# Kernel optimization log

Measured on AMD Instinct MI355X. Metric: run time of the kernel, lower is better.

## Reference

```python
import jax, jax.numpy as jnp
import numpy as np

B, N, K = 4, 8192, 24
D_POINTS, D_MODEL, PE_DIM = 32, 64, 60


def _sincos_embed(pos, embed_dim):
    # 3D sincos embedding: embed_dim//3 dims per axis, half sin half cos.
    d = embed_dim // 3                                   # 20 per axis
    omega = 1.0 / (10000.0 ** (jnp.arange(d // 2, dtype=jnp.float32) / (d / 2.0)))
    ang = pos[..., None] * omega                         # [..., 3, d//2]
    emb = jnp.concatenate([jnp.sin(ang), jnp.cos(ang)], axis=-1)  # [..., 3, d]
    return emb.reshape(pos.shape[:-1] + (embed_dim,))    # [..., 60]


def _knn_idx(xyz, k):
    # squared pairwise distances [B,N,N]; top_k(-d) == argsort(d)[:k]
    sq = jnp.sum(xyz * xyz, axis=-1)
    dists = sq[:, :, None] + sq[:, None, :] - 2.0 * jnp.einsum('bnc,bmc->bnm', xyz, xyz)
    _, idx = jax.lax.top_k(-dists, k)
    return idx                                           # [B,N,K] int32


def _gather(points, idx):
    # index_points: points [B,N,C], idx [B,N,K] -> [B,N,K,C]
    return jax.vmap(lambda p, i: p[i])(points, idx)


def setup_inputs():
    key = jax.random.key(0)
    ks = jax.random.split(key, 12)
    s = 0.02
    DK = D_MODEL * K
    return {
        'features': jax.random.normal(ks[0], (B, N, D_POINTS), jnp.float32),
        'xyz': jax.random.uniform(ks[1], (B, N, 3), jnp.float32),
        'W1': jax.random.normal(ks[2], (D_MODEL, D_POINTS), jnp.float32) * s,
        'b1': jnp.zeros((D_MODEL,), jnp.float32),
        'W2': jax.random.normal(ks[3], (D_MODEL, D_MODEL), jnp.float32) * s,
        'b2': jnp.zeros((D_MODEL,), jnp.float32),
        'Wd1': jax.random.normal(ks[4], (D_MODEL, PE_DIM), jnp.float32) * s,
        'bd1': jnp.zeros((D_MODEL,), jnp.float32),
        'Wd2': jax.random.normal(ks[5], (D_MODEL, D_MODEL), jnp.float32) * s,
        'bd2': jnp.zeros((D_MODEL,), jnp.float32),
        'Wa': jax.random.normal(ks[6], (DK, DK), jnp.float32) * s,
        'ba': jnp.zeros((DK,), jnp.float32),
    }


def reference(features, xyz, W1, b1, W2, b2, Wd1, bd1, Wd2, bd2, Wa, ba):
    knn_idx = _knn_idx(xyz, K)                # no-grad in original
    knn_xyz = _gather(xyz, knn_idx)           # [B,N,K,3]
    x = features @ W1.T + b1                  # fc1 -> [B,N,D]
    q = x
    kf = _gather(x, knn_idx)                  # [B,N,K,D]
    vf = kf
    g_xyz = xyz[:, :, None, :] - knn_xyz      # [B,N,K,3]
    pe = _sincos_embed(g_xyz, PE_DIM)         # [B,N,K,60]
    pos_enc = jnp.maximum(pe @ Wd1.T + bd1, 0.0) @ Wd2.T + bd2  # fc_delta
    pre = (q[:, :, None, :] - kf + pos_enc).reshape(B, N, K * D_MODEL)
    attn = (pre @ Wa.T + ba).reshape(B, N, K, D_MODEL)          # fc_atten
    attn = jax.nn.softmax(attn / np.float32(np.sqrt(D_MODEL)), axis=-2)
    res = jnp.einsum('bmnf,bmnf->bmf', attn, vf + pos_enc)
    res = res @ W2.T + b2 + x                 # fc2 + residual
    return res, attn
```

## Files before the change

kernel.cpp:

```cpp
#include <hip/hip_runtime.h>
#include <hip/hip_bf16.h>
#include <stdint.h>

#define BATCH 4
#define NPTS  8192
#define KNN   24
#define DPT   32
#define DM    64
#define PED   60
#define DK    (DM*KNN)
#define ROWS  (BATCH*NPTS)

#define GRIDN 16
#define NCELL (GRIDN*GRIDN*GRIDN)
#define CH    0.0625f

typedef __attribute__((ext_vector_type(8))) short short8;
typedef __attribute__((ext_vector_type(4))) float f32x4;
typedef __attribute__((address_space(3))) unsigned lds_u32;
typedef const __attribute__((address_space(1))) unsigned gbl_u32;

#define WSYNC() __builtin_amdgcn_wave_barrier()

static __device__ __forceinline__ unsigned short f2bf(float f) {
  __hip_bfloat16 h = __float2bfloat16(f);
  return *(unsigned short*)&h;
}
static __device__ __forceinline__ float bf2f(unsigned short u) {
  return __uint_as_float(((unsigned)u) << 16);
}

static __device__ __forceinline__ int cell_coord(float p) {
  int c = (int)(p * (float)GRIDN);
  c = (c < 0) ? 0 : c;
  c = (c > GRIDN - 1) ? GRIDN - 1 : c;
  return c;
}

__global__ __launch_bounds__(256) void fc1_kernel(
    const float* __restrict__ f, const float* __restrict__ W1,
    const float* __restrict__ b1, float* __restrict__ x) {
  int gid = blockIdx.x * 256 + threadIdx.x;
  int n = gid >> 6, c = gid & 63;
  const float* fr = f + (size_t)n * DPT;
  const float* wr = W1 + c * DPT;
  float acc = b1[c];
#pragma unroll
  for (int i = 0; i < DPT; ++i) acc = fmaf(fr[i], wr[i], acc);
  x[(size_t)n * DM + c] = acc;
}

__global__ __launch_bounds__(256) void grid_build_kernel(
    const float* __restrict__ xyz, int* __restrict__ cellStart,
    int* __restrict__ sortedIdx) {
  __shared__ int cnt[NCELL];
  __shared__ int partial[256];
  int b = blockIdx.x, tid = threadIdx.x;
  const float* P = xyz + (size_t)b * NPTS * 3;

  for (int i = tid; i < NCELL; i += 256) cnt[i] = 0;
  __syncthreads();
  for (int i = tid; i < NPTS; i += 256) {
    int cx = cell_coord(P[3 * i + 0]);
    int cy = cell_coord(P[3 * i + 1]);
    int cz = cell_coord(P[3 * i + 2]);
    atomicAdd(&cnt[(cx << 8) | (cy << 4) | cz], 1);
  }
  __syncthreads();
  int base = tid * 16, s = 0;
#pragma unroll
  for (int j = 0; j < 16; ++j) s += cnt[base + j];
  partial[tid] = s;
  __syncthreads();
  if (tid == 0) {
    int acc = 0;
    for (int i = 0; i < 256; ++i) { int v = partial[i]; partial[i] = acc; acc += v; }
  }
  __syncthreads();
  int acc = partial[tid];
#pragma unroll
  for (int j = 0; j < 16; ++j) {
    int c = cnt[base + j];
    cnt[base + j] = acc;
    cellStart[b * (NCELL + 1) + base + j] = acc;
    acc += c;
  }
  if (tid == 255) cellStart[b * (NCELL + 1) + NCELL] = NPTS;
  __syncthreads();
  for (int i = tid; i < NPTS; i += 256) {
    int cx = cell_coord(P[3 * i + 0]);
    int cy = cell_coord(P[3 * i + 1]);
    int cz = cell_coord(P[3 * i + 2]);
    int pos = atomicAdd(&cnt[(cx << 8) | (cy << 4) | cz], 1);
    sortedIdx[b * NPTS + pos] = i;
  }
}

__global__ __launch_bounds__(64) void grid_knn_kernel(
    const float* __restrict__ xyz, const int* __restrict__ cellStart,
    const int* __restrict__ sortedIdx, int* __restrict__ knn) {
  int t = blockIdx.x * 64 + threadIdx.x;
  int b = t >> 13, j = t & 8191;
  const int* cs = cellStart + b * (NCELL + 1);
  const int* si = sortedIdx + b * NPTS;
  const float* P = xyz + (size_t)b * NPTS * 3;

  int q = si[j];
  int n = (b << 13) + q;
  float qx = P[3 * q + 0], qy = P[3 * q + 1], qz = P[3 * q + 2];
  int cx = cell_coord(qx), cy = cell_coord(qy), cz = cell_coord(qz);

  unsigned long long key[KNN];
#pragma unroll
  for (int o = 0; o < KNN; ++o) key[o] = 0x7F800000FFFFFFFFULL;
  float lim = __builtin_inff();

  for (int rho = 0; rho <= GRIDN - 1; ++rho) {
    for (int dz = -rho; dz <= rho; ++dz) {
      int iz = cz + dz;
      if ((unsigned)iz >= GRIDN) continue;
      bool zface = (dz == -rho) || (dz == rho);
      for (int dy = -rho; dy <= rho; ++dy) {
        int iy = cy + dy;
        if ((unsigned)iy >= GRIDN) continue;
        bool face = zface || (dy == -rho) || (dy == rho);
        int dxstep = (rho == 0 || face) ? 1 : (2 * rho);
        for (int dx = -rho; dx <= rho; dx += dxstep) {
          int ix = cx + dx;
          if ((unsigned)ix >= GRIDN) continue;
          float bx = ix * CH, by = iy * CH, bz = iz * CH;
          float ex = fmaxf(fmaxf(bx - qx, qx - (bx + CH)), 0.f);
          float ey = fmaxf(fmaxf(by - qy, qy - (by + CH)), 0.f);
          float ez = fmaxf(fmaxf(bz - qz, qz - (bz + CH)), 0.f);
          float dsq = ex * ex + ey * ey + ez * ez;
          if (dsq * 0.99999f >= lim) continue;
          int cid = (ix << 8) | (iy << 4) | iz;
          int s0 = cs[cid], s1 = cs[cid + 1];
          for (int ii = s0; ii < s1; ++ii) {
            int m = si[ii];
            float ddx = qx - P[3 * m + 0];
            float ddy = qy - P[3 * m + 1];
            float ddz = qz - P[3 * m + 2];
            double dd = (double)ddx * (double)ddx + (double)ddy * (double)ddy
                      + (double)ddz * (double)ddz;
            float df = (float)dd;
            if (df < lim) {
              unsigned long long v =
                  ((unsigned long long)__float_as_uint(df) << 32) | (unsigned)m;
#pragma unroll
              for (int tt = 0; tt < KNN; ++tt) {
                bool take = v < key[tt];
                unsigned long long old = key[tt];
                key[tt] = take ? v : key[tt];
                v = take ? old : v;
              }
              lim = __uint_as_float((unsigned)(key[KNN - 1] >> 32));
            }
          }
        }
      }
    }
    float rb = rho * CH;
    if (lim < rb * rb * 0.999999f) break;
  }
#pragma unroll
  for (int o = 0; o < KNN; ++o)
    knn[(size_t)n * KNN + o] = (int)(unsigned)key[o];
}

__device__ __forceinline__ float pe_elem(int t, float gx, float gy, float gz) {
  const float OM[10] = {1.0f, 0.3981071705534972f, 0.15848931924611134f,
                        0.06309573444801933f, 0.025118864315095794f, 0.01f,
                        0.003981071705534973f, 0.001584893192461114f,
                        0.0006309573444801933f, 0.00025118864315095795f};
  int a = t / 20, r = t % 20;
  float g = (a == 0) ? gx : ((a == 1) ? gy : gz);
  float ang = g * OM[r % 10];
  return (r < 10) ? __sinf(ang) : __cosf(ang);
}

static __device__ __forceinline__ void pe_fill(
    unsigned short* scr, const float* __restrict__ xyz, const int* idxArr,
    int base, float qx, float qy, float qz, int ln) {
  for (int k = 0; k < KNN; ++k) {
    int gidx = base + idxArr[k];
    float gx = qx - xyz[(size_t)gidx * 3 + 0];
    float gy = qy - xyz[(size_t)gidx * 3 + 1];
    float gz = qz - xyz[(size_t)gidx * 3 + 2];
    float v = (ln < PED) ? pe_elem(ln, gx, gy, gz) : 0.f;
    scr[(k * 64 + ln) ^ ((k & 7) << 3)] = f2bf(v);
  }
#pragma unroll
  for (int k = KNN; k < 32; ++k)
    scr[(k * 64 + ln) ^ ((k & 7) << 3)] = 0;
  WSYNC();
}

static __device__ __forceinline__ short8 lds_read8(const unsigned short* p) {
  return *(const short8*)p;
}

static __device__ __forceinline__ void mlp_wave(
    unsigned short* scr, const unsigned short* w1b, const unsigned short* w2b,
    const float* __restrict__ bd1, const float* __restrict__ bd2, int ln) {
  int lrow = ln & 15, lq = ln >> 4;
  short8 af[2][2], bfr[4][2];
  f32x4 acc[2][4];

#pragma unroll
  for (int mt = 0; mt < 2; ++mt)
#pragma unroll
    for (int ks = 0; ks < 2; ++ks) {
      int row = mt * 16 + lrow;
      af[mt][ks] = lds_read8(scr + ((row * 64 + ks * 32 + lq * 8) ^ ((row & 7) << 3)));
    }
#pragma unroll
  for (int nt = 0; nt < 4; ++nt)
#pragma unroll
    for (int ks = 0; ks < 2; ++ks) {
      int row = nt * 16 + lrow;
      bfr[nt][ks] = lds_read8(w1b + ((row * 64 + ks * 32 + lq * 8) ^ ((row & 7) << 3)));
    }
#pragma unroll
  for (int mt = 0; mt < 2; ++mt)
#pragma unroll
    for (int nt = 0; nt < 4; ++nt) {
      f32x4 a = (f32x4){0.f, 0.f, 0.f, 0.f};
      a = __builtin_amdgcn_mfma_f32_16x16x32_bf16(af[mt][0], bfr[nt][0], a, 0, 0, 0);
      a = __builtin_amdgcn_mfma_f32_16x16x32_bf16(af[mt][1], bfr[nt][1], a, 0, 0, 0);
      acc[mt][nt] = a;
    }
  WSYNC();
#pragma unroll
  for (int mt = 0; mt < 2; ++mt)
#pragma unroll
    for (int nt = 0; nt < 4; ++nt) {
      float b1v = bd1[nt * 16 + lrow];
#pragma unroll
      for (int r = 0; r < 4; ++r) {
        int row = mt * 16 + lq * 4 + r;
        int col = nt * 16 + lrow;
        scr[(row * 64 + col) ^ ((row & 7) << 3)] =
            f2bf(fmaxf(acc[mt][nt][r] + b1v, 0.f));
      }
    }
  WSYNC();
#pragma unroll
  for (int mt = 0; mt < 2; ++mt)
#pragma unroll
    for (int ks = 0; ks < 2; ++ks) {
      int row = mt * 16 + lrow;
      af[mt][ks] = lds_read8(scr + ((row * 64 + ks * 32 + lq * 8) ^ ((row & 7) << 3)));
    }
#pragma unroll
  for (int nt = 0; nt < 4; ++nt)
#pragma unroll
    for (int ks = 0; ks < 2; ++ks) {
      int row = nt * 16 + lrow;
      bfr[nt][ks] = lds_read8(w2b + ((row * 64 + ks * 32 + lq * 8) ^ ((row & 7) << 3)));
    }
#pragma unroll
  for (int mt = 0; mt < 2; ++mt)
#pragma unroll
    for (int nt = 0; nt < 4; ++nt) {
      f32x4 a = (f32x4){0.f, 0.f, 0.f, 0.f};
      a = __builtin_amdgcn_mfma_f32_16x16x32_bf16(af[mt][0], bfr[nt][0], a, 0, 0, 0);
      a = __builtin_amdgcn_mfma_f32_16x16x32_bf16(af[mt][1], bfr[nt][1], a, 0, 0, 0);
      acc[mt][nt] = a;
    }
  WSYNC();
#pragma unroll
  for (int mt = 0; mt < 2; ++mt)
#pragma unroll
    for (int nt = 0; nt < 4; ++nt) {
      float b2v = bd2[nt * 16 + lrow];
#pragma unroll
      for (int r = 0; r < 4; ++r) {
        int row = mt * 16 + lq * 4 + r;
        int col = nt * 16 + lrow;
        scr[row * 68 + col] = f2bf(acc[mt][nt][r] + b2v);
      }
    }
  WSYNC();
}

__global__ __launch_bounds__(256) void prebuild_kernel(
    const float* __restrict__ xyz, const float* __restrict__ x,
    const int* __restrict__ knn,
    const float* __restrict__ Wd1, const float* __restrict__ bd1,
    const float* __restrict__ Wd2, const float* __restrict__ bd2,
    unsigned short* __restrict__ preOut, unsigned short* __restrict__ P16) {
  __shared__ unsigned short sW1b[4096];
  __shared__ unsigned short sW2bb[4096];
  __shared__ unsigned short sScr[4][2176];
  __shared__ int sIdx[4][KNN];
  int tid = threadIdx.x, w = tid >> 6, ln = tid & 63;
  int n = blockIdx.x * 4 + w, b = n >> 13;

  for (int q = tid; q < 4096; q += 256) {
    int row = q >> 6, kk = q & 63;
    int idx = q ^ ((row & 7) << 3);
    sW1b[idx] = (kk < PED) ? f2bf(Wd1[row * PED + kk]) : (unsigned short)0;
    sW2bb[idx] = f2bf(Wd2[q]);
  }
  if (ln < KNN) sIdx[w][ln] = knn[(size_t)n * KNN + ln];
  __syncthreads();

  float qx = xyz[(size_t)n * 3], qy = xyz[(size_t)n * 3 + 1], qz = xyz[(size_t)n * 3 + 2];
  float xq = x[(size_t)n * DM + ln];
  unsigned short* scr = &sScr[w][0];

  pe_fill(scr, xyz, &sIdx[w][0], b << 13, qx, qy, qz, ln);
  mlp_wave(scr, sW1b, sW2bb, bd1, bd2, ln);

  for (int k = 0; k < KNN; ++k) {
    int gidx = (b << 13) + sIdx[w][k];
    float kfv = x[(size_t)gidx * DM + ln];
    float p = bf2f(scr[k * 68 + ln]);
    preOut[((size_t)n * KNN + k) * DM + ln] = f2bf(xq - kfv + p);
  }
  if (P16) {
    unsigned short* pd = P16 + (size_t)n * 3072 + 1536;
#pragma unroll
    for (int k = 0; k < KNN; ++k) pd[k * 64 + ln] = scr[k * 68 + ln];
  }
}

__global__ __launch_bounds__(256) void conv_bf16_kernel(
    const float* __restrict__ src, unsigned short* __restrict__ dst, int n4) {
  int i = blockIdx.x * 256 + threadIdx.x;
  if (i < n4) {
    float4 v = ((const float4*)src)[i];
    ushort4 o;
    o.x = f2bf(v.x); o.y = f2bf(v.y); o.z = f2bf(v.z); o.w = f2bf(v.w);
    ((ushort4*)dst)[i] = o;
  }
}

__global__ __launch_bounds__(256) void copy16_kernel(
    const uint4* __restrict__ src, uint4* __restrict__ dst, int nvec) {
  int i = blockIdx.x * 256 + threadIdx.x;
  if (i < nvec) dst[i] = src[i];
}

__global__ __launch_bounds__(256) void gemm_bf16_kernel(
    const unsigned short* __restrict__ A,
    const unsigned short* __restrict__ B,
    const float* __restrict__ ba,
    unsigned short* __restrict__ Cb) {
  __shared__ unsigned short sA[8 * 512];
  __shared__ unsigned short sB[8 * 512];
  unsigned nwg = gridDim.x, orig = blockIdx.x;
  unsigned xcd = orig & 7u, qd = nwg >> 3, rr = nwg & 7u;
  unsigned wgid = (xcd < rr ? xcd * (qd + 1) : rr * (qd + 1) + (xcd - rr) * qd)
                + (orig >> 3);
  int mt = wgid / 12, nt = wgid % 12;
  int m0 = mt * 128, n0 = nt * 128;
  int tid = threadIdx.x, w = tid >> 6, L = tid & 63;
  int wr = w >> 1, wc = w & 1;
  int lrow = L & 15, lq = L >> 4;

  f32x4 acc[4][4];
#pragma unroll
  for (int i = 0; i < 4; ++i)
#pragma unroll
    for (int j = 0; j < 4; ++j) acc[i][j] = (f32x4){0.f, 0.f, 0.f, 0.f};

  for (int kt = 0; kt < DK; kt += 32) {
#pragma unroll
    for (int i = 0; i < 2; ++i) {
      int tb = w * 2 + i;
      const unsigned short* ga = A + ((size_t)(m0 + tb * 16 + lrow)) * DK + kt + lq * 8;
      __builtin_amdgcn_global_load_lds((gbl_u32*)ga, (lds_u32*)(sA + tb * 512), 16, 0, 0);
      const unsigned short* gb = B + ((size_t)(n0 + tb * 16 + lrow)) * DK + kt + lq * 8;
      __builtin_amdgcn_global_load_lds((gbl_u32*)gb, (lds_u32*)(sB + tb * 512), 16, 0, 0);
    }
    __syncthreads();
    short8 af[4], bf[4];
#pragma unroll
    for (int i = 0; i < 4; ++i)
      af[i] = *(const short8*)(sA + ((wr * 4 + i) * 64 + L) * 8);
#pragma unroll
    for (int j = 0; j < 4; ++j)
      bf[j] = *(const short8*)(sB + ((wc * 4 + j) * 64 + L) * 8);
#pragma unroll
    for (int i = 0; i < 4; ++i)
#pragma unroll
      for (int j = 0; j < 4; ++j)
        acc[i][j] = __builtin_amdgcn_mfma_f32_16x16x32_bf16(af[i], bf[j], acc[i][j], 0, 0, 0);
    __syncthreads();
  }
#pragma unroll
  for (int j = 0; j < 4; ++j) {
    int col = n0 + (wc * 4 + j) * 16 + lrow;
    float bav = ba[col];
#pragma unroll
    for (int i = 0; i < 4; ++i) {
      int rbase = m0 + (wr * 4 + i) * 16 + lq * 4;
#pragma unroll
      for (int r = 0; r < 4; ++r)
        Cb[(size_t)(rbase + r) * 3072 + col] = f2bf(acc[i][j][r] + bav);
    }
  }
}

__global__ __launch_bounds__(256) void finish_kernel(
    const float* __restrict__ x, const int* __restrict__ knn,
    const float* __restrict__ W2, const float* __restrict__ b2,
    const unsigned short* attn16, float* attnF, float* __restrict__ res) {
  __shared__ float sW2f[DM][DM + 1];
  __shared__ float sRes[4][64];
  __shared__ int sIdx[4][KNN];
  int tid = threadIdx.x, w = tid >> 6, ln = tid & 63;
  int n = blockIdx.x * 4 + w, b = n >> 13;

  for (int q = tid; q < DM * DM; q += 256) sW2f[q >> 6][q & 63] = W2[q];
  if (ln < KNN) sIdx[w][ln] = knn[(size_t)n * KNN + ln];
  __syncthreads();

  const unsigned short* lrow = attn16 + (size_t)n * 3072;
  float L[KNN], Pv[KNN];
#pragma unroll
  for (int k = 0; k < KNN; ++k) L[k] = bf2f(lrow[k * 64 + ln]);
#pragma unroll
  for (int k = 0; k < KNN; ++k) Pv[k] = bf2f(lrow[1536 + k * 64 + ln]);
  asm volatile("" ::: "memory");

  float mx = -__builtin_inff();
#pragma unroll
  for (int k = 0; k < KNN; ++k) mx = fmaxf(mx, L[k]);
  float ssum = 0.f;
#pragma unroll
  for (int k = 0; k < KNN; ++k) { L[k] = __expf((L[k] - mx) * 0.125f); ssum += L[k]; }
  float inv = 1.0f / ssum;
#pragma unroll
  for (int k = 0; k < KNN; ++k) {
    L[k] *= inv;
    attnF[(size_t)n * DK + k * 64 + ln] = L[k];
  }

  float racc = 0.f;
  for (int k = 0; k < KNN; ++k) {
    int gidx = (b << 13) + sIdx[w][k];
    float xv = x[(size_t)gidx * DM + ln];
    racc = fmaf(L[k], xv + Pv[k], racc);
  }
  sRes[w][ln] = racc;
  WSYNC();
  float oacc = b2[ln] + x[(size_t)n * DM + ln];
#pragma unroll
  for (int o = 0; o < DM; ++o) oacc = fmaf(sRes[w][o], sW2f[ln][o], oacc);
  res[(size_t)n * DM + ln] = oacc;
}

__global__ __launch_bounds__(256) void finish_full_kernel(
    const float* __restrict__ xyz, const float* __restrict__ x,
    const int* __restrict__ knn,
    const float* __restrict__ Wd1, const float* __restrict__ bd1,
    const float* __restrict__ Wd2, const float* __restrict__ bd2,
    const float* __restrict__ W2, const float* __restrict__ b2,
    const unsigned short* attn16, float* attnF, float* __restrict__ res) {
  __shared__ unsigned short sW1b[4096];
  __shared__ unsigned short sW2bb[4096];
  __shared__ float sW2f[DM][DM + 1];
  __shared__ unsigned short sScr[4][2176];
  __shared__ float sRes[4][64];
  __shared__ int sIdx[4][KNN];
  int tid = threadIdx.x, w = tid >> 6, ln = tid & 63;
  int n = blockIdx.x * 4 + w, b = n >> 13;

  for (int q = tid; q < 4096; q += 256) {
    int row = q >> 6, kk = q & 63;
    int idx = q ^ ((row & 7) << 3);
    sW1b[idx] = (kk < PED) ? f2bf(Wd1[row * PED + kk]) : (unsigned short)0;
    sW2bb[idx] = f2bf(Wd2[q]);
  }
  for (int q = tid; q < DM * DM; q += 256) sW2f[q >> 6][q & 63] = W2[q];
  if (ln < KNN) sIdx[w][ln] = knn[(size_t)n * KNN + ln];
  __syncthreads();

  float qx = xyz[(size_t)n * 3], qy = xyz[(size_t)n * 3 + 1], qz = xyz[(size_t)n * 3 + 2];
  unsigned short* scr = &sScr[w][0];
  pe_fill(scr, xyz, &sIdx[w][0], b << 13, qx, qy, qz, ln);
  mlp_wave(scr, sW1b, sW2bb, bd1, bd2, ln);

  const unsigned short* lrow = attn16 + (size_t)n * 3072;
  float L[KNN];
#pragma unroll
  for (int k = 0; k < KNN; ++k) L[k] = bf2f(lrow[k * 64 + ln]);
  asm volatile("" ::: "memory");
  float mx = -__builtin_inff();
#pragma unroll
  for (int k = 0; k < KNN; ++k) mx = fmaxf(mx, L[k]);
  float ssum = 0.f;
#pragma unroll
  for (int k = 0; k < KNN; ++k) { L[k] = __expf((L[k] - mx) * 0.125f); ssum += L[k]; }
  float inv = 1.0f / ssum;
#pragma unroll
  for (int k = 0; k < KNN; ++k) {
    L[k] *= inv;
    attnF[(size_t)n * DK + k * 64 + ln] = L[k];
  }
  float racc = 0.f;
  for (int k = 0; k < KNN; ++k) {
    int gidx = (b << 13) + sIdx[w][k];
    float xv = x[(size_t)gidx * DM + ln];
    racc = fmaf(L[k], xv + bf2f(scr[k * 68 + ln]), racc);
  }
  sRes[w][ln] = racc;
  WSYNC();
  float oacc = b2[ln] + x[(size_t)n * DM + ln];
#pragma unroll
  for (int o = 0; o < DM; ++o) oacc = fmaf(sRes[w][o], sW2f[ln][o], oacc);
  res[(size_t)n * DM + ln] = oacc;
}

extern "C" void kernel_launch(void* const* d_in, const int* in_sizes, int n_in,
                              void* d_out, int out_size, void* d_ws, size_t ws_size,
                              hipStream_t stream) {
  const float* features = (const float*)d_in[0];
  const float* xyz = (const float*)d_in[1];
  const float* W1  = (const float*)d_in[2];
  const float* b1  = (const float*)d_in[3];
  const float* W2  = (const float*)d_in[4];
  const float* b2  = (const float*)d_in[5];
  const float* Wd1 = (const float*)d_in[6];
  const float* bd1 = (const float*)d_in[7];
  const float* Wd2 = (const float*)d_in[8];
  const float* bd2 = (const float*)d_in[9];
  const float* Wa  = (const float*)d_in[10];
  const float* ba  = (const float*)d_in[11];

  float* res  = (float*)d_out;
  float* attn = (float*)d_out + (size_t)ROWS * DM;
  unsigned short* attn16 = (unsigned short*)attn;

  size_t xB   = (size_t)ROWS * DM * 4;
  size_t WaB  = (size_t)DK * DK * 2;
  size_t used = xB + (size_t)ROWS * KNN * 4;
  float* xbuf = (float*)d_ws;
  int*   knn  = (int*)((char*)d_ws + xB);

  size_t avail = (ws_size > used) ? ws_size - used : 0;
  size_t rowB = (size_t)DK * 2;
  bool bigws = avail >= WaB + (size_t)ROWS * rowB;

  int* gridCS = (int*)attn;
  int* gridSI = gridCS + BATCH * (NCELL + 1);

  hipLaunchKernelGGL(fc1_kernel, dim3(ROWS * DM / 256), dim3(256), 0, stream,
                     features, W1, b1, xbuf);
  hipLaunchKernelGGL(grid_build_kernel, dim3(BATCH), dim3(256), 0, stream,
                     xyz, gridCS, gridSI);
  hipLaunchKernelGGL(grid_knn_kernel, dim3(ROWS / 64), dim3(64), 0, stream,
                     xyz, gridCS, gridSI, knn);

  if (bigws) {
    unsigned short* WaBf = (unsigned short*)((char*)d_ws + used);
    unsigned short* preW = (unsigned short*)((char*)d_ws + used + WaB);
    hipLaunchKernelGGL(prebuild_kernel, dim3(ROWS / 4), dim3(256), 0, stream,
                       xyz, xbuf, knn, Wd1, bd1, Wd2, bd2, preW, attn16);
    {
      int n4 = DK * DK / 4;
      hipLaunchKernelGGL(conv_bf16_kernel, dim3((n4 + 255) / 256), dim3(256), 0, stream,
                         Wa, WaBf, n4);
    }
    hipLaunchKernelGGL(gemm_bf16_kernel, dim3((ROWS / 128) * 12), dim3(256), 0, stream,
                       preW, WaBf, ba, attn16);
    hipLaunchKernelGGL(finish_kernel, dim3(ROWS / 4), dim3(256), 0, stream,
                       xbuf, knn, W2, b2, attn16, attn, res);
  } else {
    unsigned short* WaBf  = (unsigned short*)d_out;
    unsigned short* chunk = (unsigned short*)((char*)d_out + WaB);
    int chunk_rows = (int)((xB - WaB) / rowB) & ~127;
    hipLaunchKernelGGL(prebuild_kernel, dim3(ROWS / 4), dim3(256), 0, stream,
                       xyz, xbuf, knn, Wd1, bd1, Wd2, bd2, attn16,
                       (unsigned short*)nullptr);
    {
      int n4 = DK * DK / 4;
      hipLaunchKernelGGL(conv_bf16_kernel, dim3((n4 + 255) / 256), dim3(256), 0, stream,
                         Wa, WaBf, n4);
    }
    {
      int cr0 = (chunk_rows < ROWS) ? chunk_rows : ROWS;
      int nvec = cr0 * (DK * 2 / 16);
      hipLaunchKernelGGL(copy16_kernel, dim3((nvec + 255) / 256), dim3(256), 0, stream,
                         (const uint4*)attn16, (uint4*)chunk, nvec);
    }
    int top = ((ROWS - 1) / chunk_rows) * chunk_rows;
    for (int r0 = top; r0 >= 0; r0 -= chunk_rows) {
      int cr = (ROWS - r0 < chunk_rows) ? (ROWS - r0) : chunk_rows;
      const unsigned short* Aptr =
          (r0 == 0) ? chunk : attn16 + (size_t)r0 * DK;
      hipLaunchKernelGGL(gemm_bf16_kernel, dim3((cr / 128) * 12), dim3(256), 0, stream,
                         Aptr, WaBf, ba, attn16 + (size_t)r0 * 3072);
    }
    hipLaunchKernelGGL(finish_full_kernel, dim3(ROWS / 4), dim3(256), 0, stream,
                       xyz, xbuf, knn, Wd1, bd1, Wd2, bd2, W2, b2,
                       attn16, attn, res);
  }
}
```

Baseline: 1.048 ms.

## Split KNN cell scan across two threads per query; triple-buffer GEMM loads

The grid KNN kernel now assigns two threads to each query point. Each thread scans alternating neighbour cells and keeps its own top-24 list, and the two sorted lists are merged through shared memory at the end. Separately, the bf16 GEMM moves from a single LDS buffer with two barriers per k-step to a 3-stage ring. Global-to-LDS loads are issued two steps ahead and waited on with vmcnt, leaving one barrier per step. The KNN split adds parallelism but weakens pruning, because each half only sees its own limit, and it uses a lot of LDS (48KB of keys per block), which may lower occupancy.

```diff
diff --git a/kernel.cpp b/kernel.cpp
--- a/kernel.cpp
+++ b/kernel.cpp
@@ -96,10 +96,13 @@
   }
 }
 
-__global__ __launch_bounds__(64) void grid_knn_kernel(
+__global__ __launch_bounds__(256) void grid_knn_kernel(
     const float* __restrict__ xyz, const int* __restrict__ cellStart,
     const int* __restrict__ sortedIdx, int* __restrict__ knn) {
-  int t = blockIdx.x * 64 + threadIdx.x;
+  __shared__ unsigned long long sKeys[256][KNN];
+  int tid = threadIdx.x;
+  int ql = tid & 127, s = tid >> 7;
+  int t = blockIdx.x * 128 + ql;
   int b = t >> 13, j = t & 8191;
   const int* cs = cellStart + b * (NCELL + 1);
   const int* si = sortedIdx + b * NPTS;
@@ -114,6 +117,7 @@
 #pragma unroll
   for (int o = 0; o < KNN; ++o) key[o] = 0x7F800000FFFFFFFFULL;
   float lim = __builtin_inff();
+  int par = 0;
 
   for (int rho = 0; rho <= GRIDN - 1; ++rho) {
     for (int dz = -rho; dz <= rho; ++dz) {
@@ -128,6 +132,9 @@
         for (int dx = -rho; dx <= rho; dx += dxstep) {
           int ix = cx + dx;
           if ((unsigned)ix >= GRIDN) continue;
+          int mine = ((par & 1) == s);
+          ++par;
+          if (!mine) continue;
           float bx = ix * CH, by = iy * CH, bz = iz * CH;
           float ex = fmaxf(fmaxf(bx - qx, qx - (bx + CH)), 0.f);
           float ey = fmaxf(fmaxf(by - qy, qy - (by + CH)), 0.f);
@@ -164,8 +171,18 @@
     if (lim < rb * rb * 0.999999f) break;
   }
 #pragma unroll
-  for (int o = 0; o < KNN; ++o)
-    knn[(size_t)n * KNN + o] = (int)(unsigned)key[o];
+  for (int o = 0; o < KNN; ++o) sKeys[tid][o] = key[o];
+  __syncthreads();
+  if (tid < 128) {
+    int i = 0, jj = 0;
+    for (int o = 0; o < KNN; ++o) {
+      unsigned long long a = sKeys[tid][i];
+      unsigned long long c = sKeys[tid + 128][jj];
+      bool ta = a < c;
+      knn[(size_t)n * KNN + o] = (int)(unsigned)(ta ? a : c);
+      if (ta) ++i; else ++jj;
+    }
+  }
 }
 
 __device__ __forceinline__ float pe_elem(int t, float gx, float gy, float gz) {
@@ -348,8 +365,8 @@
     const unsigned short* __restrict__ B,
     const float* __restrict__ ba,
     unsigned short* __restrict__ Cb) {
-  __shared__ unsigned short sA[8 * 512];
-  __shared__ unsigned short sB[8 * 512];
+  __shared__ unsigned short sA[3][4096];
+  __shared__ unsigned short sB[3][4096];
   unsigned nwg = gridDim.x, orig = blockIdx.x;
   unsigned xcd = orig & 7u, qd = nwg >> 3, rr = nwg & 7u;
   unsigned wgid = (xcd < rr ? xcd * (qd + 1) : rr * (qd + 1) + (xcd - rr) * qd)
@@ -360,36 +377,56 @@
   int wr = w >> 1, wc = w & 1;
   int lrow = L & 15, lq = L >> 4;
 
+  const unsigned short* gA0 = A + (size_t)(m0 + (w * 2) * 16 + lrow) * DK + lq * 8;
+  const unsigned short* gB0 = B + (size_t)(n0 + (w * 2) * 16 + lrow) * DK + lq * 8;
+
   f32x4 acc[4][4];
 #pragma unroll
   for (int i = 0; i < 4; ++i)
 #pragma unroll
     for (int j = 0; j < 4; ++j) acc[i][j] = (f32x4){0.f, 0.f, 0.f, 0.f};
 
-  for (int kt = 0; kt < DK; kt += 32) {
-#pragma unroll
-    for (int i = 0; i < 2; ++i) {
-      int tb = w * 2 + i;
-      const unsigned short* ga = A + ((size_t)(m0 + tb * 16 + lrow)) * DK + kt + lq * 8;
-      __builtin_amdgcn_global_load_lds((gbl_u32*)ga, (lds_u32*)(sA + tb * 512), 16, 0, 0);
-      const unsigned short* gb = B + ((size_t)(n0 + tb * 16 + lrow)) * DK + kt + lq * 8;
-      __builtin_amdgcn_global_load_lds((gbl_u32*)gb, (lds_u32*)(sB + tb * 512), 16, 0, 0);
-    }
-    __syncthreads();
-    short8 af[4], bf[4];
+#define STAGE(buf, kt)                                                        \
+  {                                                                           \
+    __builtin_amdgcn_global_load_lds((gbl_u32*)(gA0 + (kt)),                  \
+        (lds_u32*)(&sA[(buf)][(w * 2) * 512]), 16, 0, 0);                     \
+    __builtin_amdgcn_global_load_lds((gbl_u32*)(gB0 + (kt)),                  \
+        (lds_u32*)(&sB[(buf)][(w * 2) * 512]), 16, 0, 0);                     \
+    __builtin_amdgcn_global_load_lds((gbl_u32*)(gA0 + (size_t)16 * DK + (kt)),\
+        (lds_u32*)(&sA[(buf)][(w * 2 + 1) * 512]), 16, 0, 0);                 \
+    __builtin_amdgcn_global_load_lds((gbl_u32*)(gB0 + (size_t)16 * DK + (kt)),\
+        (lds_u32*)(&sB[(buf)][(w * 2 + 1) * 512]), 16, 0, 0);                 \
+  }
+
+  STAGE(0, 0);
+  STAGE(1, 32);
+
+  const int nk = DK / 32;
+  for (int ki = 0; ki < nk; ++ki) {
+    int cur = ki % 3;
+    if (ki + 1 < nk) {
+      asm volatile("s_waitcnt vmcnt(4)" ::: "memory");
+    } else {
+      asm volatile("s_waitcnt vmcnt(0)" ::: "memory");
+    }
+    __builtin_amdgcn_s_barrier();
+    asm volatile("" ::: "memory");
+    if (ki + 2 < nk) STAGE((ki + 2) % 3, (ki + 2) * 32);
+    short8 af[4], bf4[4];
 #pragma unroll
     for (int i = 0; i < 4; ++i)
-      af[i] = *(const short8*)(sA + ((wr * 4 + i) * 64 + L) * 8);
+      af[i] = *(const short8*)(&sA[cur][((wr * 4 + i) * 64 + L) * 8]);
 #pragma unroll
     for (int j = 0; j < 4; ++j)
-      bf[j] = *(const short8*)(sB + ((wc * 4 + j) * 64 + L) * 8);
+      bf4[j] = *(const short8*)(&sB[cur][((wc * 4 + j) * 64 + L) * 8]);
 #pragma unroll
     for (int i = 0; i < 4; ++i)
 #pragma unroll
       for (int j = 0; j < 4; ++j)
-        acc[i][j] = __builtin_amdgcn_mfma_f32_16x16x32_bf16(af[i], bf[j], acc[i][j], 0, 0, 0);
-    __syncthreads();
-  }
+        acc[i][j] = __builtin_amdgcn_mfma_f32_16x16x32_bf16(af[i], bf4[j], acc[i][j], 0, 0, 0);
+  }
+#undef STAGE
+
 #pragma unroll
   for (int j = 0; j < 4; ++j) {
     int col = n0 + (wc * 4 + j) * 16 + lrow;
@@ -552,7 +589,7 @@
                      features, W1, b1, xbuf);
   hipLaunchKernelGGL(grid_build_kernel, dim3(BATCH), dim3(256), 0, stream,
                      xyz, gridCS, gridSI);
-  hipLaunchKernelGGL(grid_knn_kernel, dim3(ROWS / 64), dim3(64), 0, stream,
+  hipLaunchKernelGGL(grid_knn_kernel, dim3(ROWS / 128), dim3(256), 0, stream,
                      xyz, gridCS, gridSI, knn);
 
   if (bigws) {
```

New measurement: 1.203 ms. +14.8%, slower.
